# Kernel optimization log

Hardware: AMD Instinct MI355X
Metric: run time of the kernel (lower is better)

## Reference

```python
import jax, jax.numpy as jnp
import numpy as np

N_NODES = 10000
N_EDGES = 160000
F_IN, D, DEPTH, F_OUT = 6, 512, 10, 1


def setup_inputs() -> dict:
    key = jax.random.key(0)
    ks = jax.random.split(key, 10)
    features = jax.random.normal(ks[0], (N_NODES, F_IN), dtype=jnp.float32)
    src = jax.random.randint(ks[1], (N_EDGES,), 0, N_NODES, dtype=jnp.int32)
    dst = jax.random.randint(ks[2], (N_EDGES,), 0, N_NODES, dtype=jnp.int32)
    s_in = 1.0 / np.sqrt(F_IN)
    s_h = 1.0 / np.sqrt(D)
    W_in = jax.random.uniform(ks[3], (F_IN, D), jnp.float32, -s_in, s_in)
    b_in = jax.random.uniform(ks[4], (D,), jnp.float32, -s_in, s_in)
    Ws = jax.random.uniform(ks[5], (DEPTH, D, D), jnp.float32, -s_h, s_h)
    bs = jax.random.uniform(ks[6], (DEPTH, D), jnp.float32, -s_h, s_h)
    W_out = jax.random.uniform(ks[7], (D, F_OUT), jnp.float32, -s_h, s_h)
    b_out = jax.random.uniform(ks[8], (F_OUT,), jnp.float32, -s_h, s_h)
    return {"features": features, "W_in": W_in, "b_in": b_in, "Ws": Ws,
            "bs": bs, "W_out": W_out, "b_out": b_out, "src": src, "dst": dst}


def reference(features, W_in, b_in, Ws, bs, W_out, b_out, src, dst):
    n = features.shape[0]
    # GCNLayer: aggregate = scatter-sum of neighbor features (copy_src + sum), then Linear
    agg = jax.ops.segment_sum(features[src], dst, num_segments=n)  # [N, F_in]
    x = jax.nn.relu(agg @ W_in + b_in)  # ReLU only after input layer (per forward)

    def step(x, wb):
        W, b = wb
        a = jax.ops.segment_sum(x[src], dst, num_segments=n)  # [N, D]
        return a @ W + b, None  # no activation between hidden GCN layers

    x, _ = jax.lax.scan(step, x, (Ws, bs))
    return x @ W_out + b_out  # [N, 1]
```

## Files before the change

### kernel.cpp

```cpp
#include <hip/hip_runtime.h>


#define N_NODES 10000
#define N_EDGES 160000
#define DEPTH   10

#define NB_G 40
#define NB_C 33
#define NB   (NB_G + NB_C)
#define BT   1024
#define NTHG (NB_G * BT)
#define NPB  250
#define ECAP 8192

typedef unsigned long long u64;

__device__ __forceinline__ int ldAi(const int* p) {
    return __hip_atomic_load(p, __ATOMIC_RELAXED, __HIP_MEMORY_SCOPE_AGENT);
}
__device__ __forceinline__ void stAi(int* p, int v) {
    __hip_atomic_store(p, v, __ATOMIC_RELAXED, __HIP_MEMORY_SCOPE_AGENT);
}
__device__ __forceinline__ void stAf(float* p, float v) {
    __hip_atomic_store(p, v, __ATOMIC_RELAXED, __HIP_MEMORY_SCOPE_AGENT);
}
__device__ __forceinline__ u64 ld8(const u64* p) {
    return __hip_atomic_load(p, __ATOMIC_RELAXED, __HIP_MEMORY_SCOPE_AGENT);
}
__device__ __forceinline__ void st8(u64* p, u64 v) {
    __hip_atomic_store(p, v, __ATOMIC_RELAXED, __HIP_MEMORY_SCOPE_AGENT);
}
__device__ __forceinline__ u64 packf(float f) {
    union { float f; unsigned u; } c; c.f = f;
    return (1ull << 32) | (u64)c.u;
}
__device__ __forceinline__ float unpackf(u64 v) {
    union { unsigned u; float f; } c; c.u = (unsigned)v;
    return c.f;
}
#define READY(v) ((unsigned)((v) >> 32) != 0u)

__device__ __forceinline__ float pollf(const u64* p) {
    u64 v = ld8(p);
    while (!READY(v)) { __builtin_amdgcn_s_sleep(1); v = ld8(p); }
    return unpackf(v);
}

__device__ __forceinline__ void gbar40(int* flags, int bx, int target) {
    asm volatile("s_waitcnt vmcnt(0)" ::: "memory");
    __syncthreads();
    if (threadIdx.x == 0) stAi(&flags[bx * 32], target);
    if (threadIdx.x < NB_G && threadIdx.x != bx) {
        while (ldAi(&flags[threadIdx.x * 32]) < target) __builtin_amdgcn_s_sleep(1);
    }
    __syncthreads();
}

extern "C" __global__ void __launch_bounds__(BT, 1) gcn_mega(
    const float* __restrict__ features, const float* __restrict__ W_in,
    const float* __restrict__ b_in, const float* __restrict__ Ws,
    const float* __restrict__ bs, const float* __restrict__ W_out,
    const float* __restrict__ b_out, const int* __restrict__ src,
    const int* __restrict__ dst, float* __restrict__ out,
    int* g_arrive, int* deg_done, int* scan_done, u64* gamma8, u64* vslab,
    int* deg, u64* esrc8, int* row_ptr, int* cursor, float* rslab)
{
    __shared__ int   lds_e[ECAP];
    __shared__ float s_Wb[4096];
    __shared__ float s_vt[512];
    __shared__ float s_gam[16];
    __shared__ int   s_info[2];
    __shared__ int   s_wsum[16];

    const int tx = threadIdx.x;
    const int bx = blockIdx.x;

    if (bx >= NB_G) {
        const int gi   = bx - NB_G;
        const int cw   = gi * (BT / 64) + (tx >> 6);
        const int lane = tx & 63;
        if (cw > 512) return;
        for (int s = 0; s < DEPTH; s++) {
            const int l = 9 - s;
            const float* rowp = (cw < 512)
                ? (Ws + (size_t)l * (512 * 512) + (size_t)cw * 512)
                : (bs + (size_t)l * 512);
            float wrow[8];
#pragma unroll
            for (int c = 0; c < 8; c++) wrow[c] = rowp[lane + 64 * c];
            float vin[8];
            if (s == 0) {
#pragma unroll
                for (int c = 0; c < 8; c++) vin[c] = W_out[lane + 64 * c];
            } else {
                const u64* vb = vslab + (size_t)s * 512;
                u64 raw[8];
#pragma unroll
                for (int c = 0; c < 8; c++) raw[c] = ld8(vb + lane + 64 * c);
                for (;;) {
                    bool ok = true;
#pragma unroll
                    for (int c = 0; c < 8; c++)
                        if (!READY(raw[c])) { ok = false; raw[c] = ld8(vb + lane + 64 * c); }
                    if (ok) break;
                    __builtin_amdgcn_s_sleep(1);
                }
#pragma unroll
                for (int c = 0; c < 8; c++) vin[c] = unpackf(raw[c]);
            }
            float acc = 0.f;
#pragma unroll
            for (int c = 0; c < 8; c++) acc += wrow[c] * vin[c];
#pragma unroll
            for (int off = 32; off; off >>= 1) acc += __shfl_xor(acc, off, 64);
            if (lane == 0) {
                if (cw < 512) st8(vslab + (size_t)(s + 1) * 512 + cw, packf(acc));
                else          st8(gamma8 + l, packf(acc));
            }
        }
        return;
    }


    {
        const int t0 = bx * BT + tx;
        for (int e = t0; e < N_EDGES; e += NTHG) atomicAdd(&deg[dst[e]], 1);
    }
    for (int idx = tx; idx < 4096; idx += BT) {
        int j = idx >> 3, k = idx & 7;
        float v = 0.f;
        if (k < 6) v = W_in[k * 512 + j];
        else if (k == 6) v = b_in[j];
        s_Wb[idx] = v;
    }
    asm volatile("s_waitcnt vmcnt(0)" ::: "memory");
    __syncthreads();
    if (tx == 0) stAi(&deg_done[bx * 32], 1);

    if (bx == 0) {
        if (tx < NB_G) {
            while (ldAi(&deg_done[tx * 32]) < 1) __builtin_amdgcn_s_sleep(1);
        }
        __syncthreads();
        const int lane = tx & 63, wid = tx >> 6;
        const bool sact = tx < 1000;
        int lv[10];
        int ssum = 0;
        if (sact) {
#pragma unroll
            for (int i = 0; i < 10; i++) { lv[i] = ldAi(&deg[tx * 10 + i]); ssum += lv[i]; }
        }
        int v = ssum;
#pragma unroll
        for (int off = 1; off < 64; off <<= 1) {
            int u = __shfl_up(v, off, 64);
            if (lane >= off) v += u;
        }
        if (lane == 63) s_wsum[wid] = v;
        __syncthreads();
        if (wid == 0) {
            int w = (lane < 16) ? s_wsum[lane] : 0;
#pragma unroll
            for (int off = 1; off < 16; off <<= 1) {
                int u = __shfl_up(w, off, 64);
                if (lane >= off) w += u;
            }
            if (lane < 16) s_wsum[lane] = w;
        }
        __syncthreads();
        if (sact) {
            int run = (wid ? s_wsum[wid - 1] : 0) + (v - ssum);
#pragma unroll
            for (int i = 0; i < 10; i++) {
                stAi(&row_ptr[tx * 10 + i], run);
                stAi(&cursor[tx * 10 + i], run);
                run += lv[i];
            }
            if (tx == 999) stAi(&row_ptr[N_NODES], run);
        }
        asm volatile("s_waitcnt vmcnt(0)" ::: "memory");
        __syncthreads();
        if (tx == 0) stAi(scan_done, 1);
    } else {
        if (tx == 0) {
            while (ldAi(scan_done) < 1) __builtin_amdgcn_s_sleep(1);
        }
        __syncthreads();
    }

    {
        const int t0 = bx * BT + tx;
        for (int e = t0; e < N_EDGES; e += NTHG) {
            int d = dst[e];
            unsigned sv = (unsigned)src[e];
            int pos = atomicAdd(&cursor[d], 1);
            st8(&esrc8[pos], (1ull << 32) | (u64)sv);
        }
    }

    if (tx == 0) {
        s_info[0] = ldAi(&row_ptr[bx * NPB]);
        s_info[1] = ldAi(&row_ptr[bx * NPB + NPB]);
    }
    __syncthreads();
    const int e_lo = s_info[0];
    const int slen = s_info[1] - e_lo;
    const bool use_lds = (slen <= ECAP);
    if (use_lds) {
        for (int i = tx; i < slen; i += BT) {
            u64 v = ld8(&esrc8[e_lo + i]);
            while (!READY(v)) { __builtin_amdgcn_s_sleep(1); v = ld8(&esrc8[e_lo + i]); }
            lds_e[i] = (int)(unsigned)v;
        }
    }
    __syncthreads();

    const int node = bx * NPB + (tx >> 2);
    const int sub  = tx & 3;
    const bool act = tx < 4 * NPB;
    int ns = 0, ne = 0;
    float a0 = 0.f, a1 = 0.f, a2 = 0.f, a3 = 0.f, a4 = 0.f, a5 = 0.f;
    if (act) {
        ns = ldAi(&row_ptr[node]);
        ne = ldAi(&row_ptr[node + 1]);
        for (int pp = ns + sub; pp < ne; pp += 4) {
            int j;
            if (use_lds) j = lds_e[pp - e_lo];
            else {
                u64 v = ld8(&esrc8[pp]);
                while (!READY(v)) { __builtin_amdgcn_s_sleep(1); v = ld8(&esrc8[pp]); }
                j = (int)(unsigned)v;
            }
            const float2* f = (const float2*)(features + (size_t)j * 6);
            float2 f0 = f[0], f1 = f[1], f2 = f[2];
            a0 += f0.x; a1 += f0.y; a2 += f1.x;
            a3 += f1.y; a4 += f2.x; a5 += f2.y;
        }
        a0 += __shfl_xor(a0, 1, 64); a0 += __shfl_xor(a0, 2, 64);
        a1 += __shfl_xor(a1, 1, 64); a1 += __shfl_xor(a1, 2, 64);
        a2 += __shfl_xor(a2, 1, 64); a2 += __shfl_xor(a2, 2, 64);
        a3 += __shfl_xor(a3, 1, 64); a3 += __shfl_xor(a3, 2, 64);
        a4 += __shfl_xor(a4, 1, 64); a4 += __shfl_xor(a4, 2, 64);
        a5 += __shfl_xor(a5, 1, 64); a5 += __shfl_xor(a5, 2, 64);
    }

    if (tx < 512) s_vt[tx] = pollf(vslab + 10 * 512 + tx);
    else if (tx < 512 + DEPTH) s_gam[tx - 512] = pollf(gamma8 + (tx - 512));
    __syncthreads();

    if (act) {
        const float4* Wb4 = (const float4*)s_Wb;
        float zacc = 0.f;
#pragma unroll 4
        for (int jj = 0; jj < 128; jj++) {
            int j = (jj << 2) | sub;
            float4 wA = Wb4[2 * j];
            float4 wB = Wb4[2 * j + 1];
            float tv = wB.z + a0 * wA.x + a1 * wA.y + a2 * wA.z +
                       a3 * wA.w + a4 * wB.x + a5 * wB.y;
            zacc += fmaxf(tv, 0.f) * s_vt[j];
        }
        zacc += __shfl_xor(zacc, 1, 64);
        zacc += __shfl_xor(zacc, 2, 64);
        if (sub == 0) stAf(&rslab[node], zacc);
    }
    int gt = 1;
    gbar40(g_arrive, bx, gt++);

    for (int l = 0; l < DEPTH; l++) {
        if (act) {
            const float* rin = rslab + (size_t)l * N_NODES;
            float h0 = 0.f, h1 = 0.f, h2 = 0.f, h3 = 0.f;
            int pp = ns + sub;
            if (use_lds) {
                for (; pp + 12 < ne; pp += 16) {
                    h0 += rin[lds_e[pp - e_lo]];
                    h1 += rin[lds_e[pp + 4 - e_lo]];
                    h2 += rin[lds_e[pp + 8 - e_lo]];
                    h3 += rin[lds_e[pp + 12 - e_lo]];
                }
                for (; pp < ne; pp += 4) h0 += rin[lds_e[pp - e_lo]];
            } else {
                for (; pp < ne; pp += 4) {
                    u64 ev = ld8(&esrc8[pp]);
                    while (!READY(ev)) { __builtin_amdgcn_s_sleep(1); ev = ld8(&esrc8[pp]); }
                    h0 += rin[(int)(unsigned)ev];
                }
            }
            float hs = (h0 + h1) + (h2 + h3);
            hs += __shfl_xor(hs, 1, 64);
            hs += __shfl_xor(hs, 2, 64);
            if (sub == 0) {
                float res = hs + s_gam[l];
                if (l == DEPTH - 1) out[node] = res + b_out[0];
                else stAf(&rslab[(size_t)(l + 1) * N_NODES + node], res);
            }
        }
        if (l < DEPTH - 1) gbar40(g_arrive, bx, gt++);
    }
}


extern "C" void kernel_launch(void* const* d_in, const int* in_sizes, int n_in,
                              void* d_out, int out_size, void* d_ws, size_t ws_size,
                              hipStream_t stream) {
    const float* features = (const float*)d_in[0];
    const float* W_in     = (const float*)d_in[1];
    const float* b_in     = (const float*)d_in[2];
    const float* Ws       = (const float*)d_in[3];
    const float* bs       = (const float*)d_in[4];
    const float* W_out    = (const float*)d_in[5];
    const float* b_out    = (const float*)d_in[6];
    const int*   src      = (const int*)d_in[7];
    const int*   dst      = (const int*)d_in[8];
    float* out = (float*)d_out;

    char* base = (char*)d_ws;
    int* g_arrive  = (int*)(base + 0);
    int* deg_done  = (int*)(base + 5120);
    int* scan_done = (int*)(base + 10240);
    u64* gamma8    = (u64*)(base + 10368);
    u64* vslab     = (u64*)(base + 10496);
    int* deg       = (int*)(base + 55552);
    u64* esrc8     = (u64*)(base + 95552);
    const size_t MEMSET_END = 1375552;
    int*   row_ptr = (int*)(base + 1375552);
    int*   cursor  = (int*)(base + 1415680);
    float* rslab   = (float*)(base + 1455680);

    hipMemsetAsync(base, 0, MEMSET_END, stream);

    gcn_mega<<<NB, BT, 0, stream>>>(features, W_in, b_in, Ws, bs, W_out, b_out,
                                    src, dst, out,
                                    g_arrive, deg_done, scan_done, gamma8,
                                    vslab, deg, esrc8, row_ptr, cursor, rslab);
}
```

Before: 200.4 us.

## Split persistent GCN kernel into many small 256-thread blocks with packed barrier flags

Reshapes the persistent megakernel from 73 blocks of 1024 threads to 225 blocks of 256 threads, with 160 graph blocks of 63 nodes each and 65 weight-chain blocks where each wave now computes two matvec rows. The grid barrier packs its flags contiguously and each polling thread checks four flags, and loads from the per-layer rslab now go through relaxed atomics with a padded stride. The aim is to spread gather and weight-chain work across more compute units and cut the cost of the 1024-thread syncs. The cost is a barrier across four times as many blocks, and the scan now runs 40 serial elements per thread.

After: 212.1 us. +5.8%, slower.

```diff
diff --git a/kernel.cpp b/kernel.cpp
--- a/kernel.cpp
+++ b/kernel.cpp
@@ -5,13 +5,14 @@
 #define N_EDGES 160000
 #define DEPTH   10
 
-#define NB_G 40
-#define NB_C 33
+#define NB_G 160
+#define NB_C 65
 #define NB   (NB_G + NB_C)
-#define BT   1024
+#define BT   256
 #define NTHG (NB_G * BT)
-#define NPB  250
-#define ECAP 8192
+#define NPB  63
+#define ECAP 3072
+#define RSTRIDE 10240
 
 typedef unsigned long long u64;
 
@@ -20,6 +21,9 @@
 }
 __device__ __forceinline__ void stAi(int* p, int v) {
     __hip_atomic_store(p, v, __ATOMIC_RELAXED, __HIP_MEMORY_SCOPE_AGENT);
+}
+__device__ __forceinline__ float ldAf(const float* p) {
+    return __hip_atomic_load(p, __ATOMIC_RELAXED, __HIP_MEMORY_SCOPE_AGENT);
 }
 __device__ __forceinline__ void stAf(float* p, float v) {
     __hip_atomic_store(p, v, __ATOMIC_RELAXED, __HIP_MEMORY_SCOPE_AGENT);
@@ -46,12 +50,22 @@
     return unpackf(v);
 }
 
-__device__ __forceinline__ void gbar40(int* flags, int bx, int target) {
+__device__ __forceinline__ void gbar(int* flags, int bx, int target) {
     asm volatile("s_waitcnt vmcnt(0)" ::: "memory");
     __syncthreads();
-    if (threadIdx.x == 0) stAi(&flags[bx * 32], target);
-    if (threadIdx.x < NB_G && threadIdx.x != bx) {
-        while (ldAi(&flags[threadIdx.x * 32]) < target) __builtin_amdgcn_s_sleep(1);
+    const int tx = threadIdx.x;
+    if (tx == 0) stAi(&flags[bx], target);
+    if (tx < 40) {
+        const int b0 = tx * 4;
+        int f0 = ldAi(&flags[b0]),     f1 = ldAi(&flags[b0 + 1]);
+        int f2 = ldAi(&flags[b0 + 2]), f3 = ldAi(&flags[b0 + 3]);
+        while (f0 < target || f1 < target || f2 < target || f3 < target) {
+            __builtin_amdgcn_s_sleep(1);
+            if (f0 < target) f0 = ldAi(&flags[b0]);
+            if (f1 < target) f1 = ldAi(&flags[b0 + 1]);
+            if (f2 < target) f2 = ldAi(&flags[b0 + 2]);
+            if (f3 < target) f3 = ldAi(&flags[b0 + 3]);
+        }
     }
     __syncthreads();
 }
@@ -70,24 +84,33 @@
     __shared__ float s_vt[512];
     __shared__ float s_gam[16];
     __shared__ int   s_info[2];
-    __shared__ int   s_wsum[16];
+    __shared__ int   s_wsum[4];
 
     const int tx = threadIdx.x;
     const int bx = blockIdx.x;
 
     if (bx >= NB_G) {
-        const int gi   = bx - NB_G;
-        const int cw   = gi * (BT / 64) + (tx >> 6);
+        const int cw   = (bx - NB_G) * 4 + (tx >> 6);
         const int lane = tx & 63;
-        if (cw > 512) return;
+        const int j0 = cw, j1 = cw + 260;
+        if (j0 > 512) return;
+        const bool two = (j1 <= 512);
         for (int s = 0; s < DEPTH; s++) {
             const int l = 9 - s;
-            const float* rowp = (cw < 512)
-                ? (Ws + (size_t)l * (512 * 512) + (size_t)cw * 512)
+            const float* r0 = (j0 < 512)
+                ? (Ws + (size_t)l * (512 * 512) + (size_t)j0 * 512)
                 : (bs + (size_t)l * 512);
-            float wrow[8];
-#pragma unroll
-            for (int c = 0; c < 8; c++) wrow[c] = rowp[lane + 64 * c];
+            float w0[8];
+#pragma unroll
+            for (int c = 0; c < 8; c++) w0[c] = r0[lane + 64 * c];
+            float w1[8];
+            if (two) {
+                const float* r1 = (j1 < 512)
+                    ? (Ws + (size_t)l * (512 * 512) + (size_t)j1 * 512)
+                    : (bs + (size_t)l * 512);
+#pragma unroll
+                for (int c = 0; c < 8; c++) w1[c] = r1[lane + 64 * c];
+            }
             float vin[8];
             if (s == 0) {
 #pragma unroll
@@ -108,14 +131,24 @@
 #pragma unroll
                 for (int c = 0; c < 8; c++) vin[c] = unpackf(raw[c]);
             }
-            float acc = 0.f;
-#pragma unroll
-            for (int c = 0; c < 8; c++) acc += wrow[c] * vin[c];
-#pragma unroll
-            for (int off = 32; off; off >>= 1) acc += __shfl_xor(acc, off, 64);
+            float a0 = 0.f, a1 = 0.f;
+#pragma unroll
+            for (int c = 0; c < 8; c++) {
+                a0 += w0[c] * vin[c];
+                if (two) a1 += w1[c] * vin[c];
+            }
+#pragma unroll
+            for (int off = 32; off; off >>= 1) {
+                a0 += __shfl_xor(a0, off, 64);
+                if (two) a1 += __shfl_xor(a1, off, 64);
+            }
             if (lane == 0) {
-                if (cw < 512) st8(vslab + (size_t)(s + 1) * 512 + cw, packf(acc));
-                else          st8(gamma8 + l, packf(acc));
+                if (j0 < 512) st8(vslab + (size_t)(s + 1) * 512 + j0, packf(a0));
+                else          st8(gamma8 + l, packf(a0));
+                if (two) {
+                    if (j1 < 512) st8(vslab + (size_t)(s + 1) * 512 + j1, packf(a1));
+                    else          st8(gamma8 + l, packf(a1));
+                }
             }
         }
         return;
@@ -135,20 +168,30 @@
     }
     asm volatile("s_waitcnt vmcnt(0)" ::: "memory");
     __syncthreads();
-    if (tx == 0) stAi(&deg_done[bx * 32], 1);
+    if (tx == 0) stAi(&deg_done[bx], 1);
 
     if (bx == 0) {
-        if (tx < NB_G) {
-            while (ldAi(&deg_done[tx * 32]) < 1) __builtin_amdgcn_s_sleep(1);
+        if (tx < 40) {
+            const int b0 = tx * 4;
+            int f0 = ldAi(&deg_done[b0]),     f1 = ldAi(&deg_done[b0 + 1]);
+            int f2 = ldAi(&deg_done[b0 + 2]), f3 = ldAi(&deg_done[b0 + 3]);
+            while (!(f0 & f1 & f2 & f3)) {
+                __builtin_amdgcn_s_sleep(1);
+                if (!f0) f0 = ldAi(&deg_done[b0]);
+                if (!f1) f1 = ldAi(&deg_done[b0 + 1]);
+                if (!f2) f2 = ldAi(&deg_done[b0 + 2]);
+                if (!f3) f3 = ldAi(&deg_done[b0 + 3]);
+            }
         }
         __syncthreads();
         const int lane = tx & 63, wid = tx >> 6;
-        const bool sact = tx < 1000;
-        int lv[10];
+        const int base = tx * 40;
+        const bool sact = base < N_NODES;
+        int lv[40];
         int ssum = 0;
         if (sact) {
 #pragma unroll
-            for (int i = 0; i < 10; i++) { lv[i] = ldAi(&deg[tx * 10 + i]); ssum += lv[i]; }
+            for (int i = 0; i < 40; i++) { lv[i] = ldAi(&deg[base + i]); ssum += lv[i]; }
         }
         int v = ssum;
 #pragma unroll
@@ -159,24 +202,24 @@
         if (lane == 63) s_wsum[wid] = v;
         __syncthreads();
         if (wid == 0) {
-            int w = (lane < 16) ? s_wsum[lane] : 0;
-#pragma unroll
-            for (int off = 1; off < 16; off <<= 1) {
+            int w = (lane < 4) ? s_wsum[lane] : 0;
+#pragma unroll
+            for (int off = 1; off < 4; off <<= 1) {
                 int u = __shfl_up(w, off, 64);
                 if (lane >= off) w += u;
             }
-            if (lane < 16) s_wsum[lane] = w;
+            if (lane < 4) s_wsum[lane] = w;
         }
         __syncthreads();
         if (sact) {
             int run = (wid ? s_wsum[wid - 1] : 0) + (v - ssum);
 #pragma unroll
-            for (int i = 0; i < 10; i++) {
-                stAi(&row_ptr[tx * 10 + i], run);
-                stAi(&cursor[tx * 10 + i], run);
+            for (int i = 0; i < 40; i++) {
+                stAi(&row_ptr[base + i], run);
+                stAi(&cursor[base + i], run);
                 run += lv[i];
             }
-            if (tx == 999) stAi(&row_ptr[N_NODES], run);
+            if (tx == 249) stAi(&row_ptr[N_NODES], run);
         }
         asm volatile("s_waitcnt vmcnt(0)" ::: "memory");
         __syncthreads();
@@ -198,9 +241,11 @@
         }
     }
 
+    const int lo_node = (bx * NPB < N_NODES) ? bx * NPB : N_NODES;
+    const int hi_node = (bx * NPB + NPB < N_NODES) ? bx * NPB + NPB : N_NODES;
     if (tx == 0) {
-        s_info[0] = ldAi(&row_ptr[bx * NPB]);
-        s_info[1] = ldAi(&row_ptr[bx * NPB + NPB]);
+        s_info[0] = ldAi(&row_ptr[lo_node]);
+        s_info[1] = ldAi(&row_ptr[hi_node]);
     }
     __syncthreads();
     const int e_lo = s_info[0];
@@ -217,7 +262,7 @@
 
     const int node = bx * NPB + (tx >> 2);
     const int sub  = tx & 3;
-    const bool act = tx < 4 * NPB;
+    const bool act = (tx < 4 * NPB) && (node < N_NODES);
     int ns = 0, ne = 0;
     float a0 = 0.f, a1 = 0.f, a2 = 0.f, a3 = 0.f, a4 = 0.f, a5 = 0.f;
     if (act) {
@@ -244,8 +289,9 @@
         a5 += __shfl_xor(a5, 1, 64); a5 += __shfl_xor(a5, 2, 64);
     }
 
-    if (tx < 512) s_vt[tx] = pollf(vslab + 10 * 512 + tx);
-    else if (tx < 512 + DEPTH) s_gam[tx - 512] = pollf(gamma8 + (tx - 512));
+    s_vt[tx]       = pollf(vslab + 10 * 512 + tx);
+    s_vt[tx + 256] = pollf(vslab + 10 * 512 + tx + 256);
+    if (tx < DEPTH) s_gam[tx] = pollf(gamma8 + tx);
     __syncthreads();
 
     if (act) {
@@ -265,26 +311,26 @@
         if (sub == 0) stAf(&rslab[node], zacc);
     }
     int gt = 1;
-    gbar40(g_arrive, bx, gt++);
+    gbar(g_arrive, bx, gt++);
 
     for (int l = 0; l < DEPTH; l++) {
         if (act) {
-            const float* rin = rslab + (size_t)l * N_NODES;
+            const float* rin = rslab + (size_t)l * RSTRIDE;
             float h0 = 0.f, h1 = 0.f, h2 = 0.f, h3 = 0.f;
             int pp = ns + sub;
             if (use_lds) {
                 for (; pp + 12 < ne; pp += 16) {
-                    h0 += rin[lds_e[pp - e_lo]];
-                    h1 += rin[lds_e[pp + 4 - e_lo]];
-                    h2 += rin[lds_e[pp + 8 - e_lo]];
-                    h3 += rin[lds_e[pp + 12 - e_lo]];
+                    h0 += ldAf(&rin[lds_e[pp - e_lo]]);
+                    h1 += ldAf(&rin[lds_e[pp + 4 - e_lo]]);
+                    h2 += ldAf(&rin[lds_e[pp + 8 - e_lo]]);
+                    h3 += ldAf(&rin[lds_e[pp + 12 - e_lo]]);
                 }
-                for (; pp < ne; pp += 4) h0 += rin[lds_e[pp - e_lo]];
+                for (; pp < ne; pp += 4) h0 += ldAf(&rin[lds_e[pp - e_lo]]);
             } else {
                 for (; pp < ne; pp += 4) {
                     u64 ev = ld8(&esrc8[pp]);
                     while (!READY(ev)) { __builtin_amdgcn_s_sleep(1); ev = ld8(&esrc8[pp]); }
-                    h0 += rin[(int)(unsigned)ev];
+                    h0 += ldAf(&rin[(int)(unsigned)ev]);
                 }
             }
             float hs = (h0 + h1) + (h2 + h3);
@@ -293,10 +339,10 @@
             if (sub == 0) {
                 float res = hs + s_gam[l];
                 if (l == DEPTH - 1) out[node] = res + b_out[0];
-                else stAf(&rslab[(size_t)(l + 1) * N_NODES + node], res);
-            }
-        }
-        if (l < DEPTH - 1) gbar40(g_arrive, bx, gt++);
+                else stAf(&rslab[(size_t)(l + 1) * RSTRIDE + node], res);
+            }
+        }
+        if (l < DEPTH - 1) gbar(g_arrive, bx, gt++);
     }
 }
 
@@ -317,16 +363,16 @@
 
     char* base = (char*)d_ws;
     int* g_arrive  = (int*)(base + 0);
-    int* deg_done  = (int*)(base + 5120);
-    int* scan_done = (int*)(base + 10240);
-    u64* gamma8    = (u64*)(base + 10368);
-    u64* vslab     = (u64*)(base + 10496);
-    int* deg       = (int*)(base + 55552);
-    u64* esrc8     = (u64*)(base + 95552);
-    const size_t MEMSET_END = 1375552;
-    int*   row_ptr = (int*)(base + 1375552);
-    int*   cursor  = (int*)(base + 1415680);
-    float* rslab   = (float*)(base + 1455680);
+    int* deg_done  = (int*)(base + 1024);
+    int* scan_done = (int*)(base + 2048);
+    u64* gamma8    = (u64*)(base + 2176);
+    u64* vslab     = (u64*)(base + 2304);
+    int* deg       = (int*)(base + 47360);
+    u64* esrc8     = (u64*)(base + 87424);
+    const size_t MEMSET_END = 1367424;
+    int*   row_ptr = (int*)(base + 1367424);
+    int*   cursor  = (int*)(base + 1407488);
+    float* rslab   = (float*)(base + 1447552);
 
     hipMemsetAsync(base, 0, MEMSET_END, stream);
 
```
